# Kernel tuning notes

Measured on AMD Instinct MI355X. Metric: run time of the kernel, lower is better.

## Reference

```python
import jax, jax.numpy as jnp
import numpy as np

B, N, D, H = 1024, 32, 512, 4
HD = D // H


def setup_inputs() -> dict:
    key = jax.random.key(0)
    k1, k2, k3 = jax.random.split(key, 3)
    scale = 1.0 / np.sqrt(D)  # keep logits in a sane range (mimics xavier init)
    return {
        "agent_hiddens": jax.random.normal(k1, (B, N, D), dtype=jnp.float32),
        "padding_mask": jnp.zeros((B, N), dtype=bool),
        "in_proj_weight": jax.random.normal(k2, (3 * D, D), dtype=jnp.float32) * scale,
        "in_proj_bias": jnp.zeros((3 * D,), dtype=jnp.float32),
        "out_proj_weight": jax.random.normal(k3, (D, D), dtype=jnp.float32) * scale,
        "out_proj_bias": jnp.zeros((D,), dtype=jnp.float32),
    }


def reference(agent_hiddens, padding_mask, in_proj_weight, in_proj_bias,
              out_proj_weight, out_proj_bias):
    # Equivalent to the per-agent loop: full self-attention over the N agents
    # with the diagonal (self) and padded agents masked out of the keys.
    qkv = agent_hiddens @ in_proj_weight.T + in_proj_bias      # (B, N, 3D)
    q, k, v = jnp.split(qkv, 3, axis=-1)
    # (B, H, N, HD)
    q = q.reshape(B, N, H, HD).transpose(0, 2, 1, 3)
    k = k.reshape(B, N, H, HD).transpose(0, 2, 1, 3)
    v = v.reshape(B, N, H, HD).transpose(0, 2, 1, 3)

    scores = jnp.einsum('bhqd,bhkd->bhqk', q, k) / jnp.sqrt(jnp.float32(HD))
    self_mask = jnp.eye(N, dtype=bool)                         # exclude j == i
    mask = self_mask[None, None, :, :] | padding_mask[:, None, None, :]
    scores = jnp.where(mask, -jnp.inf, scores)
    attn = jax.nn.softmax(scores, axis=-1)                     # (B, H, N, N)

    ctx = jnp.einsum('bhqk,bhkd->bhqd', attn, v)               # (B, H, N, HD)
    ctx = ctx.transpose(0, 2, 1, 3).reshape(B, N, D)
    return ctx @ out_proj_weight.T + out_proj_bias
```

## Files before the change

kernel.cpp:

```cpp
#include <hip/hip_runtime.h>
#include <hip/hip_bf16.h>


typedef __attribute__((ext_vector_type(4))) float  f32x4;
typedef __attribute__((ext_vector_type(8))) short  bf16x8;
typedef __attribute__((ext_vector_type(4))) short  bf16x4;
typedef __attribute__((ext_vector_type(4))) int    i32x4;

__device__ __forceinline__ unsigned short f2bf(float f) {
    unsigned u = __builtin_bit_cast(unsigned, f);
    u = (u + 0x7FFFu + ((u >> 16) & 1u)) >> 16;
    return (unsigned short)u;
}
__device__ __forceinline__ float bf2f(unsigned short h) {
    unsigned u = ((unsigned)h) << 16;
    return __builtin_bit_cast(float, u);
}

__device__ __forceinline__ void gload_lds16(const void* g, void* l) {
    __builtin_amdgcn_global_load_lds(
        (const __attribute__((address_space(1))) void*)g,
        (__attribute__((address_space(3))) void*)l, 16, 0, 0);
}

__global__ __launch_bounds__(256)
void cvt3_kernel(const float* __restrict__ s0, unsigned short* __restrict__ d0, int n0,
                 const float* __restrict__ s1, unsigned short* __restrict__ d1, int n1,
                 const float* __restrict__ s2, unsigned short* __restrict__ d2, int n2)
{
    int i = blockIdx.x * 256 + threadIdx.x;
    const float* s; unsigned short* d; int k;
    if (i < n0)                { s = s0; d = d0; k = i; }
    else if (i < n0 + n1)      { s = s1; d = d1; k = i - n0; }
    else if (i < n0 + n1 + n2) { s = s2; d = d2; k = i - n0 - n1; }
    else return;
    f32x4 v = ((const f32x4*)s)[k];
    bf16x4 o;
#pragma unroll
    for (int e = 0; e < 4; ++e) o[e] = (short)f2bf(v[e]);
    ((bf16x4*)d)[k] = o;
}

template<int MODE>
__global__ __launch_bounds__(256)
void gemm_bt(const unsigned short* __restrict__ A, const unsigned short* __restrict__ Bw,
             const float* __restrict__ bias, void* __restrict__ Cout, int ldc, int ntx)
{
    __shared__ unsigned short As[2][128 * 64];
    __shared__ unsigned short Bs[2][128 * 64];

    const int t = threadIdx.x;
    const int nwg = gridDim.x;
    const int cpx = nwg >> 3;
    const int lin = blockIdx.x;
    const int swz = (lin & 7) * cpx + (lin >> 3);
    const int bx = swz % ntx, by = swz / ntx;
    const int mbase = by * 128, nbase = bx * 128;

    const int w = t >> 6, l = t & 63;
    const int wr = w >> 1, wc = w & 1;
    const int lg = l >> 4, lr = l & 15;

    int soff[4];
#pragma unroll
    for (int i = 0; i < 4; ++i) {
        int p = i * 256 + t;
        int row = p >> 3, pc = p & 7;
        int lc = pc ^ (row & 7);
        soff[i] = row * 512 + lc * 8;
    }
    const unsigned short* Ab = A  + (size_t)mbase * 512;
    const unsigned short* Bb = Bw + (size_t)nbase * 512;

    f32x4 acc[4][4] = {};

    auto STAGE = [&](int buf, int ks) {
#pragma unroll
        for (int i = 0; i < 4; ++i) {
            gload_lds16(Ab + soff[i] + ks, &As[buf][(i * 256 + w * 64) * 8]);
            gload_lds16(Bb + soff[i] + ks, &Bs[buf][(i * 256 + w * 64) * 8]);
        }
    };
    auto COMPUTE = [&](int buf) {
#pragma unroll
        for (int kk = 0; kk < 64; kk += 32) {
            const int lc = (kk >> 3) + lg;
            bf16x8 af[4], bfr[4];
#pragma unroll
            for (int mi = 0; mi < 4; ++mi) {
                int r = wr * 64 + mi * 16 + lr;
                af[mi] = *(const bf16x8*)&As[buf][r * 64 + ((lc ^ (r & 7)) << 3)];
            }
#pragma unroll
            for (int ni = 0; ni < 4; ++ni) {
                int n = wc * 64 + ni * 16 + lr;
                bfr[ni] = *(const bf16x8*)&Bs[buf][n * 64 + ((lc ^ (n & 7)) << 3)];
            }
#pragma unroll
            for (int mi = 0; mi < 4; ++mi)
#pragma unroll
                for (int ni = 0; ni < 4; ++ni)
                    acc[mi][ni] = __builtin_amdgcn_mfma_f32_16x16x32_bf16(
                        af[mi], bfr[ni], acc[mi][ni], 0, 0, 0);
        }
    };

    int cur = 0;
    STAGE(0, 0);
    __syncthreads();
#pragma unroll 1
    for (int ti = 0; ti < 7; ++ti) {
        STAGE(cur ^ 1, (ti + 1) << 6);
        COMPUTE(cur);
        __syncthreads();
        cur ^= 1;
    }
    COMPUTE(cur);

#pragma unroll
    for (int ni = 0; ni < 4; ++ni) {
        int col = nbase + wc * 64 + ni * 16 + lr;
        float bv = bias[col];
#pragma unroll
        for (int mi = 0; mi < 4; ++mi) {
            int row0 = mbase + wr * 64 + mi * 16 + lg * 4;
#pragma unroll
            for (int ri = 0; ri < 4; ++ri) {
                float v = acc[mi][ni][ri] + bv;
                if (MODE == 0)
                    ((unsigned short*)Cout)[(size_t)(row0 + ri) * ldc + col] = f2bf(v);
                else
                    ((float*)Cout)[(size_t)(row0 + ri) * ldc + col] = v;
            }
        }
    }
}

__global__ __launch_bounds__(256)
void attn_kernel(const unsigned short* __restrict__ qkv,
                 const unsigned char* __restrict__ pad,
                 unsigned short* __restrict__ ctx)
{
    __shared__ f32x4 Qs[32 * 32];
    __shared__ f32x4 Ks[32 * 32];
    __shared__ f32x4 Vs[32 * 32];
    __shared__ float Ps[32 * 33];

    const int bid = blockIdx.x;
    const int b = bid >> 2, h = bid & 3;
    const int t = threadIdx.x;
    const int r = t >> 3, j = t & 7;

    const unsigned short* base = qkv + ((size_t)(b * 32 + r) * 1536 + h * 128);
#pragma unroll
    for (int sel = 0; sel < 3; ++sel) {
        f32x4* dst = (sel == 0) ? Qs : (sel == 1) ? Ks : Vs;
        const unsigned short* src = base + sel * 512 + j * 16;
#pragma unroll
        for (int it = 0; it < 2; ++it) {
            i32x4 raw = *(const i32x4*)(src + it * 8);
            float fv[8];
#pragma unroll
            for (int e = 0; e < 8; ++e) {
                unsigned word = ((const unsigned*)&raw)[e >> 1];
                unsigned short hb = (e & 1) ? (unsigned short)(word >> 16)
                                            : (unsigned short)(word & 0xffffu);
                fv[e] = bf2f(hb);
            }
            int c0 = j * 4 + it * 2;
            f32x4 v0 = {fv[0], fv[1], fv[2], fv[3]};
            f32x4 v1 = {fv[4], fv[5], fv[6], fv[7]};
            dst[r * 32 + ((c0    ) ^ r)] = v0;
            dst[r * 32 + ((c0 + 1) ^ r)] = v1;
        }
    }
    __syncthreads();

    const int q  = r;
    const int kc = j * 4;
    float s[4] = {0.f, 0.f, 0.f, 0.f};
#pragma unroll 4
    for (int d4 = 0; d4 < 32; ++d4) {
        f32x4 qv = Qs[q * 32 + (d4 ^ q)];
#pragma unroll
        for (int jj = 0; jj < 4; ++jj) {
            f32x4 kv = Ks[(kc + jj) * 32 + (d4 ^ (kc + jj))];
#pragma unroll
            for (int e = 0; e < 4; ++e) s[jj] = fmaf(qv[e], kv[e], s[jj]);
        }
    }
    const float sc = 0.08838834764831845f;
    float m = -INFINITY;
#pragma unroll
    for (int jj = 0; jj < 4; ++jj) {
        int kcol = kc + jj;
        bool msk = (kcol == q) || (pad[b * 32 + kcol] != 0);
        s[jj] = msk ? -INFINITY : s[jj] * sc;
        m = fmaxf(m, s[jj]);
    }
    m = fmaxf(m, __shfl_xor(m, 1));
    m = fmaxf(m, __shfl_xor(m, 2));
    m = fmaxf(m, __shfl_xor(m, 4));
    float p[4], sum = 0.f;
#pragma unroll
    for (int jj = 0; jj < 4; ++jj) { p[jj] = __expf(s[jj] - m); sum += p[jj]; }
    sum += __shfl_xor(sum, 1);
    sum += __shfl_xor(sum, 2);
    sum += __shfl_xor(sum, 4);
#pragma unroll
    for (int jj = 0; jj < 4; ++jj) Ps[q * 33 + kc + jj] = p[jj];
    __syncthreads();

    float c[16] = {0.f};
#pragma unroll 4
    for (int k = 0; k < 32; ++k) {
        float pv = Ps[q * 33 + k];
#pragma unroll
        for (int cc = 0; cc < 4; ++cc) {
            f32x4 vv = Vs[k * 32 + ((j + 8 * cc) ^ k)];
#pragma unroll
            for (int e = 0; e < 4; ++e) c[cc * 4 + e] = fmaf(pv, vv[e], c[cc * 4 + e]);
        }
    }
    const float inv = 1.0f / sum;
    unsigned short* co = ctx + (size_t)(b * 32 + q) * 512 + h * 128;
#pragma unroll
    for (int cc = 0; cc < 4; ++cc) {
        bf16x4 ov;
#pragma unroll
        for (int e = 0; e < 4; ++e) ov[e] = (short)f2bf(c[cc * 4 + e] * inv);
        *(bf16x4*)(co + (j + 8 * cc) * 4) = ov;
    }
}

extern "C" void kernel_launch(void* const* d_in, const int* in_sizes, int n_in,
                              void* d_out, int out_size, void* d_ws, size_t ws_size,
                              hipStream_t stream)
{
    const float*         X    = (const float*)d_in[0];
    const unsigned char* pad  = (const unsigned char*)d_in[1];
    const float*         Win  = (const float*)d_in[2];
    const float*         bin  = (const float*)d_in[3];
    const float*         Wout = (const float*)d_in[4];
    const float*         bout = (const float*)d_in[5];
    float*               out  = (float*)d_out;

    char* ws = (char*)d_ws;
    unsigned short* qkvb  = (unsigned short*)(ws);
    unsigned short* Xb    = (unsigned short*)(ws + (size_t)100663296);
    unsigned short* ctxb  = Xb;
    unsigned short* Winb  = (unsigned short*)(ws + (size_t)134217728);
    unsigned short* Woutb = (unsigned short*)(ws + (size_t)135790592);

    dim3 blk(256);
    cvt3_kernel<<<dim3(17408), blk, 0, stream>>>(X, Xb, 4194304,
                                                 Win, Winb, 196608,
                                                 Wout, Woutb, 65536);
    gemm_bt<0><<<dim3(3072), blk, 0, stream>>>(Xb, Winb, bin, qkvb, 1536, 12);
    attn_kernel<<<dim3(4096), blk, 0, stream>>>(qkvb, pad, ctxb);
    gemm_bt<1><<<dim3(1024), blk, 0, stream>>>(ctxb, Woutb, bout, out, 512, 4);
}
```

Measured before the change: 289.0 us.

## Compute attention with MFMA and produce transposed V via separate GEMM

Replaces the scalar-FMA LDS-based attention kernel with a one-wavefront-per-(batch,head) MFMA kernel. QK^T and PV now run on 32x32x16 bf16 matrix instructions, and the softmax stays in registers with cross-lane shuffles. To feed PV, the QKV projection is split: Q/K are written as before and V is computed as a transposed output (W_v · X^T) through a new GEMM mode with row bias. This removes the LDS staging, the syncs and the FP32 scalar math. In exchange it adds an extra GEMM launch, strided scattered bf16 stores for ctx, and the softmax probabilities are rounded to bf16.

```diff
diff --git a/kernel.cpp b/kernel.cpp
--- a/kernel.cpp
+++ b/kernel.cpp
@@ -2,19 +2,16 @@
 #include <hip/hip_bf16.h>
 
 
-typedef __attribute__((ext_vector_type(4))) float  f32x4;
-typedef __attribute__((ext_vector_type(8))) short  bf16x8;
-typedef __attribute__((ext_vector_type(4))) short  bf16x4;
-typedef __attribute__((ext_vector_type(4))) int    i32x4;
+typedef __attribute__((ext_vector_type(4)))  float f32x4;
+typedef __attribute__((ext_vector_type(16))) float f32x16;
+typedef __attribute__((ext_vector_type(8)))  short bf16x8;
+typedef __attribute__((ext_vector_type(4)))  short bf16x4;
+typedef __attribute__((ext_vector_type(4)))  int   i32x4;
 
 __device__ __forceinline__ unsigned short f2bf(float f) {
     unsigned u = __builtin_bit_cast(unsigned, f);
     u = (u + 0x7FFFu + ((u >> 16) & 1u)) >> 16;
     return (unsigned short)u;
-}
-__device__ __forceinline__ float bf2f(unsigned short h) {
-    unsigned u = ((unsigned)h) << 16;
-    return __builtin_bit_cast(float, u);
 }
 
 __device__ __forceinline__ void gload_lds16(const void* g, void* l) {
@@ -66,8 +63,7 @@
     for (int i = 0; i < 4; ++i) {
         int p = i * 256 + t;
         int row = p >> 3, pc = p & 7;
-        int lc = pc ^ (row & 7);
-        soff[i] = row * 512 + lc * 8;
+        soff[i] = row * 512 + (pc ^ (row & 7)) * 8;
     }
     const unsigned short* Ab = A  + (size_t)mbase * 512;
     const unsigned short* Bb = Bw + (size_t)nbase * 512;
@@ -117,119 +113,112 @@
     }
     COMPUTE(cur);
 
+    float brow[4][4];
+    if (MODE == 2) {
+#pragma unroll
+        for (int mi = 0; mi < 4; ++mi)
+#pragma unroll
+            for (int ri = 0; ri < 4; ++ri)
+                brow[mi][ri] = bias[mbase + wr * 64 + mi * 16 + lg * 4 + ri];
+    }
 #pragma unroll
     for (int ni = 0; ni < 4; ++ni) {
         int col = nbase + wc * 64 + ni * 16 + lr;
-        float bv = bias[col];
+        float bcol = (MODE == 2) ? 0.f : bias[col];
 #pragma unroll
         for (int mi = 0; mi < 4; ++mi) {
             int row0 = mbase + wr * 64 + mi * 16 + lg * 4;
 #pragma unroll
             for (int ri = 0; ri < 4; ++ri) {
-                float v = acc[mi][ni][ri] + bv;
-                if (MODE == 0)
+                float v = acc[mi][ni][ri] + ((MODE == 2) ? brow[mi][ri] : bcol);
+                if (MODE == 1)
+                    ((float*)Cout)[(size_t)(row0 + ri) * ldc + col] = v;
+                else
                     ((unsigned short*)Cout)[(size_t)(row0 + ri) * ldc + col] = f2bf(v);
-                else
-                    ((float*)Cout)[(size_t)(row0 + ri) * ldc + col] = v;
             }
         }
     }
 }
 
 __global__ __launch_bounds__(256)
-void attn_kernel(const unsigned short* __restrict__ qkv,
-                 const unsigned char* __restrict__ pad,
-                 unsigned short* __restrict__ ctx)
-{
-    __shared__ f32x4 Qs[32 * 32];
-    __shared__ f32x4 Ks[32 * 32];
-    __shared__ f32x4 Vs[32 * 32];
-    __shared__ float Ps[32 * 33];
-
-    const int bid = blockIdx.x;
-    const int b = bid >> 2, h = bid & 3;
-    const int t = threadIdx.x;
-    const int r = t >> 3, j = t & 7;
-
-    const unsigned short* base = qkv + ((size_t)(b * 32 + r) * 1536 + h * 128);
-#pragma unroll
-    for (int sel = 0; sel < 3; ++sel) {
-        f32x4* dst = (sel == 0) ? Qs : (sel == 1) ? Ks : Vs;
-        const unsigned short* src = base + sel * 512 + j * 16;
-#pragma unroll
-        for (int it = 0; it < 2; ++it) {
-            i32x4 raw = *(const i32x4*)(src + it * 8);
-            float fv[8];
-#pragma unroll
-            for (int e = 0; e < 8; ++e) {
-                unsigned word = ((const unsigned*)&raw)[e >> 1];
-                unsigned short hb = (e & 1) ? (unsigned short)(word >> 16)
-                                            : (unsigned short)(word & 0xffffu);
-                fv[e] = bf2f(hb);
-            }
-            int c0 = j * 4 + it * 2;
-            f32x4 v0 = {fv[0], fv[1], fv[2], fv[3]};
-            f32x4 v1 = {fv[4], fv[5], fv[6], fv[7]};
-            dst[r * 32 + ((c0    ) ^ r)] = v0;
-            dst[r * 32 + ((c0 + 1) ^ r)] = v1;
-        }
-    }
-    __syncthreads();
-
-    const int q  = r;
-    const int kc = j * 4;
-    float s[4] = {0.f, 0.f, 0.f, 0.f};
-#pragma unroll 4
-    for (int d4 = 0; d4 < 32; ++d4) {
-        f32x4 qv = Qs[q * 32 + (d4 ^ q)];
-#pragma unroll
-        for (int jj = 0; jj < 4; ++jj) {
-            f32x4 kv = Ks[(kc + jj) * 32 + (d4 ^ (kc + jj))];
-#pragma unroll
-            for (int e = 0; e < 4; ++e) s[jj] = fmaf(qv[e], kv[e], s[jj]);
-        }
-    }
+void attn_mfma(const unsigned short* __restrict__ qk,
+               const unsigned short* __restrict__ Vt,
+               const unsigned char* __restrict__ pad,
+               unsigned short* __restrict__ ctx)
+{
+    const int wid = blockIdx.x * 4 + (threadIdx.x >> 6);
+    const int b = wid >> 2, h = wid & 3;
+    const int l = threadIdx.x & 63;
+    const int q = l & 31;
+    const int hi = l >> 5;
+
+    const unsigned short* rowp = qk + (size_t)(b * 32 + q) * 1024 + h * 128;
+
+    f32x16 s = {};
+#pragma unroll
+    for (int st = 0; st < 8; ++st) {
+        int d0 = st * 16 + hi * 8;
+        bf16x8 kf = *(const bf16x8*)(rowp + 512 + d0);
+        bf16x8 qf = *(const bf16x8*)(rowp + d0);
+        s = __builtin_amdgcn_mfma_f32_32x32x16_bf16(kf, qf, s, 0, 0, 0);
+    }
+
+    unsigned long long bal = __ballot(pad[b * 32 + q] != 0);
+    unsigned padbits = (unsigned)bal | (unsigned)(bal >> 32);
     const float sc = 0.08838834764831845f;
+    float sv[16];
     float m = -INFINITY;
 #pragma unroll
-    for (int jj = 0; jj < 4; ++jj) {
-        int kcol = kc + jj;
-        bool msk = (kcol == q) || (pad[b * 32 + kcol] != 0);
-        s[jj] = msk ? -INFINITY : s[jj] * sc;
-        m = fmaxf(m, s[jj]);
-    }
-    m = fmaxf(m, __shfl_xor(m, 1));
-    m = fmaxf(m, __shfl_xor(m, 2));
-    m = fmaxf(m, __shfl_xor(m, 4));
-    float p[4], sum = 0.f;
-#pragma unroll
-    for (int jj = 0; jj < 4; ++jj) { p[jj] = __expf(s[jj] - m); sum += p[jj]; }
-    sum += __shfl_xor(sum, 1);
-    sum += __shfl_xor(sum, 2);
-    sum += __shfl_xor(sum, 4);
-#pragma unroll
-    for (int jj = 0; jj < 4; ++jj) Ps[q * 33 + kc + jj] = p[jj];
-    __syncthreads();
-
-    float c[16] = {0.f};
-#pragma unroll 4
-    for (int k = 0; k < 32; ++k) {
-        float pv = Ps[q * 33 + k];
-#pragma unroll
-        for (int cc = 0; cc < 4; ++cc) {
-            f32x4 vv = Vs[k * 32 + ((j + 8 * cc) ^ k)];
-#pragma unroll
-            for (int e = 0; e < 4; ++e) c[cc * 4 + e] = fmaf(pv, vv[e], c[cc * 4 + e]);
-        }
-    }
+    for (int r = 0; r < 16; ++r) {
+        int k = (r & 3) + 8 * (r >> 2) + 4 * hi;
+        bool msk = (k == q) || ((padbits >> k) & 1u);
+        sv[r] = msk ? -INFINITY : s[r] * sc;
+        m = fmaxf(m, sv[r]);
+    }
+    m = fmaxf(m, __shfl_xor(m, 32));
+    float p[16], sum = 0.f;
+#pragma unroll
+    for (int r = 0; r < 16; ++r) { p[r] = __expf(sv[r] - m); sum += p[r]; }
+    sum += __shfl_xor(sum, 32);
     const float inv = 1.0f / sum;
-    unsigned short* co = ctx + (size_t)(b * 32 + q) * 512 + h * 128;
-#pragma unroll
-    for (int cc = 0; cc < 4; ++cc) {
-        bf16x4 ov;
-#pragma unroll
-        for (int e = 0; e < 4; ++e) ov[e] = (short)f2bf(c[cc * 4 + e] * inv);
-        *(bf16x4*)(co + (j + 8 * cc) * 4) = ov;
+#pragma unroll
+    for (int r = 0; r < 16; ++r) p[r] *= inv;
+
+    bf16x8 pa[2];
+#pragma unroll
+    for (int t2 = 0; t2 < 2; ++t2) {
+        unsigned pk[4], pw[4];
+#pragma unroll
+        for (int i = 0; i < 4; ++i)
+            pk[i] = ((unsigned)f2bf(p[8 * t2 + 2 * i + 1]) << 16)
+                  |  (unsigned)f2bf(p[8 * t2 + 2 * i]);
+#pragma unroll
+        for (int i = 0; i < 4; ++i)
+            pw[i] = (unsigned)__shfl_xor((int)pk[i], 32);
+        unsigned w0 = hi ? pw[2] : pk[0];
+        unsigned w1 = hi ? pw[3] : pk[1];
+        unsigned w2 = hi ? pk[2] : pw[0];
+        unsigned w3 = hi ? pk[3] : pw[1];
+        i32x4 wv = {(int)w0, (int)w1, (int)w2, (int)w3};
+        pa[t2] = __builtin_bit_cast(bf16x8, wv);
+    }
+
+#pragma unroll
+    for (int dt = 0; dt < 4; ++dt) {
+        f32x16 c = {};
+#pragma unroll
+        for (int t2 = 0; t2 < 2; ++t2) {
+            const unsigned short* vp =
+                Vt + (size_t)(h * 128 + dt * 32 + q) * 32768 + b * 32 + t2 * 16 + hi * 8;
+            bf16x8 vb = *(const bf16x8*)vp;
+            c = __builtin_amdgcn_mfma_f32_32x32x16_bf16(pa[t2], vb, c, 0, 0, 0);
+        }
+        unsigned short* co = ctx + (size_t)(b * 32) * 512 + h * 128 + dt * 32 + q;
+#pragma unroll
+        for (int r = 0; r < 16; ++r) {
+            int qr = (r & 3) + 8 * (r >> 2) + 4 * hi;
+            co[(size_t)qr * 512] = f2bf(c[r]);
+        }
     }
 }
 
@@ -246,7 +235,8 @@
     float*               out  = (float*)d_out;
 
     char* ws = (char*)d_ws;
-    unsigned short* qkvb  = (unsigned short*)(ws);
+    unsigned short* qkb   = (unsigned short*)(ws);
+    unsigned short* Vtb   = (unsigned short*)(ws + (size_t)67108864);
     unsigned short* Xb    = (unsigned short*)(ws + (size_t)100663296);
     unsigned short* ctxb  = Xb;
     unsigned short* Winb  = (unsigned short*)(ws + (size_t)134217728);
@@ -256,7 +246,9 @@
     cvt3_kernel<<<dim3(17408), blk, 0, stream>>>(X, Xb, 4194304,
                                                  Win, Winb, 196608,
                                                  Wout, Woutb, 65536);
-    gemm_bt<0><<<dim3(3072), blk, 0, stream>>>(Xb, Winb, bin, qkvb, 1536, 12);
-    attn_kernel<<<dim3(4096), blk, 0, stream>>>(qkvb, pad, ctxb);
+    gemm_bt<0><<<dim3(2048), blk, 0, stream>>>(Xb, Winb, bin, qkb, 1024, 8);
+    gemm_bt<2><<<dim3(1024), blk, 0, stream>>>(Winb + (size_t)1024 * 512, Xb,
+                                               bin + 1024, Vtb, 32768, 256);
+    attn_mfma<<<dim3(1024), blk, 0, stream>>>(qkb, Vtb, pad, ctxb);
     gemm_bt<1><<<dim3(1024), blk, 0, stream>>>(ctxb, Woutb, bout, out, 512, 4);
 }
```

Result: faster. 257.7 us (-10.8%).
